# Kernel optimization log

Measured on AMD Instinct MI355X. Metric: run time of the kernel, lower is better.

## Reference

```python
import jax, jax.numpy as jnp
import numpy as np

N = 100000
HEADS = 4
NHID = 32


def _gat_conv(x, src, dst, W, a_src, a_dst, b):
    # x: [N, Fin]; src/dst: [E'] (self-loops already appended)
    h = (x @ W).reshape(N, HEADS, NHID)                      # [N, H, D]
    al_src = jnp.einsum('nhd,hd->nh', h, a_src)              # [N, H]
    al_dst = jnp.einsum('nhd,hd->nh', h, a_dst)
    e = jax.nn.leaky_relu(al_src[src] + al_dst[dst], 0.2)    # [E', H]
    # segment softmax over incoming edges of each destination node
    m = jax.ops.segment_max(e, dst, num_segments=N)          # [N, H]
    ex = jnp.exp(e - m[dst])
    s = jax.ops.segment_sum(ex, dst, num_segments=N)         # [N, H]
    alpha = ex / (s[dst] + 1e-16)                            # [E', H]
    msg = h[src] * alpha[:, :, None]                         # [E', H, D]
    out = jax.ops.segment_sum(msg, dst, num_segments=N)      # [N, H, D]
    return out.reshape(N, HEADS * NHID) + b


def setup_inputs() -> dict:
    key = jax.random.key(0)
    ks = jax.random.split(key, 16)
    E = 1600000
    NFEAT, NCLASS = 128, 10
    width = HEADS * NHID  # 128
    sc = 0.1
    inp = {
        'x': jax.random.normal(ks[0], (N, NFEAT), jnp.float32),
        'edge_index': jax.random.randint(ks[1], (2, E), 0, N, jnp.int64)
            if jax.config.jax_enable_x64 else jax.random.randint(ks[1], (2, E), 0, N, jnp.int32),
        'W0': jax.random.normal(ks[2], (NFEAT, width), jnp.float32) * sc,
        'a_src0': jax.random.normal(ks[3], (HEADS, NHID), jnp.float32) * sc,
        'a_dst0': jax.random.normal(ks[4], (HEADS, NHID), jnp.float32) * sc,
        'b0': jnp.zeros((width,), jnp.float32),
        'W1': jax.random.normal(ks[5], (width, width), jnp.float32) * sc,
        'a_src1': jax.random.normal(ks[6], (HEADS, NHID), jnp.float32) * sc,
        'a_dst1': jax.random.normal(ks[7], (HEADS, NHID), jnp.float32) * sc,
        'b1': jnp.zeros((width,), jnp.float32),
        'W2': jax.random.normal(ks[8], (width, width), jnp.float32) * sc,
        'a_src2': jax.random.normal(ks[9], (HEADS, NHID), jnp.float32) * sc,
        'a_dst2': jax.random.normal(ks[10], (HEADS, NHID), jnp.float32) * sc,
        'b2': jnp.zeros((width,), jnp.float32),
        'fc_W': jax.random.normal(ks[11], (width, NCLASS), jnp.float32) * sc,
        'fc_b': jnp.zeros((NCLASS,), jnp.float32),
    }
    return inp


def reference(x, edge_index, W0, a_src0, a_dst0, b0, W1, a_src1, a_dst1, b1,
              W2, a_src2, a_dst2, b2, fc_W, fc_b):
    # PyG GATConv default add_self_loops=True
    loops = jnp.arange(N, dtype=edge_index.dtype)
    src = jnp.concatenate([edge_index[0], loops])
    dst = jnp.concatenate([edge_index[1], loops])
    h = x
    for (W, a_s, a_d, b) in ((W0, a_src0, a_dst0, b0),
                             (W1, a_src1, a_dst1, b1),
                             (W2, a_src2, a_dst2, b2)):
        h = jax.nn.elu(_gat_conv(h, src, dst, W, a_s, a_d, b))
        # F.dropout(training=False) -> identity
    logits = h @ fc_W + fc_b
    return jax.nn.log_softmax(logits, axis=1)
```

## Files before the change

kernel.cpp:

```cpp
#include <hip/hip_runtime.h>
#include <math.h>

#define NN 100000
#define FEAT 128
#define NHEAD 4
#define BSH 9
#define BNODES 512
#define NBUCK 196
#define BCAP 16384
#define PA_EPT 16
#define GTILES 6250
#define GEMMB 512
#define HSTRIDE 136
#define SRCMASK 0x1FFFF

typedef unsigned int uint;
typedef unsigned short ushort;
typedef __attribute__((ext_vector_type(8))) short short8;
typedef __attribute__((ext_vector_type(4))) float fx4;

__device__ __forceinline__ float lrelu(float v) { return v > 0.f ? v : 0.2f * v; }

__device__ __forceinline__ ushort f2bf(float f) {
    uint u = __float_as_uint(f);
    return (ushort)((u + 0x7fffu + ((u >> 16) & 1u)) >> 16);
}
__device__ __forceinline__ float bf_lo(uint u) { return __uint_as_float(u << 16); }
__device__ __forceinline__ float bf_hi(uint u) { return __uint_as_float(u & 0xffff0000u); }

__device__ __forceinline__ short8 pack8f(const float* p) {
    float4 a = *(const float4*)p, b = *(const float4*)(p + 4);
    short8 v;
    v[0] = (short)f2bf(a.x); v[1] = (short)f2bf(a.y);
    v[2] = (short)f2bf(a.z); v[3] = (short)f2bf(a.w);
    v[4] = (short)f2bf(b.x); v[5] = (short)f2bf(b.y);
    v[6] = (short)f2bf(b.z); v[7] = (short)f2bf(b.w);
    return v;
}

template <bool FP32IN>
__device__ __forceinline__ void gemm_body(
    const void* __restrict__ in, const float* __restrict__ W,
    const float* __restrict__ a_src, const float* __restrict__ a_dst,
    ushort* __restrict__ hbf, float* __restrict__ al_s, float* __restrict__ al_d,
    int bid, int gridn)
{
    __shared__ __align__(16) ushort WA[FEAT * FEAT];
    __shared__ __align__(16) ushort HS[4][16 * HSTRIDE];
    const int t = threadIdx.x;
    for (int idx = t; idx < FEAT * FEAT; idx += 256) {
        int k = idx >> 7, m = idx & 127;
        int mt = m >> 4, kt = k >> 5, qq = (k >> 3) & 3, j = k & 7;
        int ln = qq * 16 + (m & 15);
        WA[((mt * 4 + kt) * 64 + ln) * 8 + j] = f2bf(W[idx]);
    }
    __syncthreads();

    const int wv = t >> 6, lane = t & 63;
    const int node_l = lane & 15, q = lane >> 4;

    short8 afr[8][4];
    #pragma unroll
    for (int mt = 0; mt < 8; ++mt)
        #pragma unroll
        for (int kt = 0; kt < 4; ++kt)
            afr[mt][kt] = *(const short8*)&WA[((mt * 4 + kt) * 64 + lane) * 8];

    const ushort* inbf = (const ushort*)in;
    const float*  inf  = (const float*)in;

    for (int tile = bid * 4 + wv; tile < GTILES; tile += gridn * 4) {
        const int n0 = tile * 16;
        short8 b0, b1, b2, b3;
        if (FP32IN) {
            const float* rf = inf + (size_t)(n0 + node_l) * FEAT + q * 8;
            b0 = pack8f(rf);
            b1 = pack8f(rf + 32);
            b2 = pack8f(rf + 64);
            b3 = pack8f(rf + 96);
        } else {
            const ushort* rowp = inbf + (size_t)(n0 + node_l) * FEAT + q * 8;
            b0 = *(const short8*)(rowp);
            b1 = *(const short8*)(rowp + 32);
            b2 = *(const short8*)(rowp + 64);
            b3 = *(const short8*)(rowp + 96);
        }
        fx4 zero = {0.f, 0.f, 0.f, 0.f};
        fx4 acc[8];
        #pragma unroll
        for (int mt = 0; mt < 8; ++mt) acc[mt] = zero;
        #pragma unroll
        for (int kt = 0; kt < 4; ++kt) {
            short8 b = (kt == 0) ? b0 : (kt == 1) ? b1 : (kt == 2) ? b2 : b3;
            #pragma unroll
            for (int mt = 0; mt < 8; ++mt)
                acc[mt] = __builtin_amdgcn_mfma_f32_16x16x32_bf16(afr[mt][kt], b, acc[mt], 0, 0, 0);
        }
        float ps[4] = {0.f, 0.f, 0.f, 0.f};
        float pd[4] = {0.f, 0.f, 0.f, 0.f};
        #pragma unroll
        for (int mt = 0; mt < 8; ++mt) {
            float4 as4 = *(const float4*)(a_src + mt * 16 + q * 4);
            float4 ad4 = *(const float4*)(a_dst + mt * 16 + q * 4);
            ps[mt >> 1] += acc[mt][0] * as4.x + acc[mt][1] * as4.y + acc[mt][2] * as4.z + acc[mt][3] * as4.w;
            pd[mt >> 1] += acc[mt][0] * ad4.x + acc[mt][1] * ad4.y + acc[mt][2] * ad4.z + acc[mt][3] * ad4.w;
            ushort4 hv;
            hv.x = f2bf(acc[mt][0]); hv.y = f2bf(acc[mt][1]);
            hv.z = f2bf(acc[mt][2]); hv.w = f2bf(acc[mt][3]);
            *(ushort4*)&HS[wv][node_l * HSTRIDE + mt * 16 + q * 4] = hv;
        }
        #pragma unroll
        for (int h = 0; h < 4; ++h) {
            ps[h] += __shfl_xor(ps[h], 16); ps[h] += __shfl_xor(ps[h], 32);
            pd[h] += __shfl_xor(pd[h], 16); pd[h] += __shfl_xor(pd[h], 32);
        }
        float vs = (q == 0) ? ps[0] : (q == 1) ? ps[1] : (q == 2) ? ps[2] : ps[3];
        float vd = (q == 0) ? pd[0] : (q == 1) ? pd[1] : (q == 2) ? pd[2] : pd[3];
        al_s[(n0 + node_l) * 4 + q] = vs;
        al_d[(n0 + node_l) * 4 + q] = vd;
        #pragma unroll
        for (int it = 0; it < 4; ++it) {
            int fi = it * 64 + lane;
            int row = fi >> 4, colc = fi & 15;
            short8 v = *(const short8*)&HS[wv][row * HSTRIDE + colc * 8];
            *(short8*)(hbf + (size_t)n0 * FEAT + (size_t)fi * 8) = v;
        }
    }
}

__device__ __forceinline__ void phaseA_body(
    const int* __restrict__ ei, int E, int* bcursor, uint* __restrict__ pairs, int bid)
{
    __shared__ int lh[NBUCK], lb[NBUCK];
    int t = threadIdx.x;
    if (t < NBUCK) lh[t] = 0;
    __syncthreads();
    int base = bid * (256 * PA_EPT) + t;
    int s[PA_EPT], d[PA_EPT];
    #pragma unroll
    for (int k = 0; k < PA_EPT; ++k) {
        int i = base + k * 256;
        if (i < E)            { s[k] = ei[i]; d[k] = ei[E + i]; }
        else if (i < E + NN)  { s[k] = i - E; d[k] = s[k]; }
        else                  { s[k] = 0; d[k] = -1; }
        if (d[k] >= 0) atomicAdd(&lh[d[k] >> BSH], 1);
    }
    __syncthreads();
    if (t < NBUCK) {
        int c = lh[t];
        lb[t] = c ? atomicAdd(&bcursor[t], c) : 0;
        lh[t] = 0;
    }
    __syncthreads();
    #pragma unroll
    for (int k = 0; k < PA_EPT; ++k) {
        if (d[k] >= 0) {
            int b = d[k] >> BSH;
            int off = atomicAdd(&lh[b], 1);
            pairs[lb[b] + off] = ((uint)(d[k] & (BNODES - 1)) << 17) | (uint)s[k];
        }
    }
}

__global__ __launch_bounds__(256, 2) void gemm_mfma_kernel(
    const void* __restrict__ in, const float* __restrict__ W,
    const float* __restrict__ a_src, const float* __restrict__ a_dst,
    ushort* __restrict__ hbf, float* __restrict__ al_s, float* __restrict__ al_d)
{
    gemm_body<false>(in, W, a_src, a_dst, hbf, al_s, al_d, blockIdx.x, GEMMB);
}

__global__ __launch_bounds__(256, 2) void gemm0_phaseA_kernel(
    const float* __restrict__ x, const float* __restrict__ W,
    const float* __restrict__ a_src, const float* __restrict__ a_dst,
    ushort* __restrict__ hbf, float* __restrict__ al_s, float* __restrict__ al_d,
    const int* __restrict__ ei, int E, int* bcursor, uint* __restrict__ pairs)
{
    if (blockIdx.x < GEMMB)
        gemm_body<true>(x, W, a_src, a_dst, hbf, al_s, al_d, blockIdx.x, GEMMB);
    else
        phaseA_body(ei, E, bcursor, pairs, blockIdx.x - GEMMB);
}


__global__ __launch_bounds__(256) void bucket_hist_kernel(
    const int* __restrict__ ei, int E, int* bsize)
{
    __shared__ int lh[NBUCK];
    int t = threadIdx.x;
    if (t < NBUCK) lh[t] = 0;
    __syncthreads();
    int stride = gridDim.x * 256;
    for (int i = blockIdx.x * 256 + t; i < E + NN; i += stride) {
        int d = (i < E) ? ei[E + i] : (i - E);
        atomicAdd(&lh[d >> BSH], 1);
    }
    __syncthreads();
    if (t < NBUCK && lh[t]) atomicAdd(&bsize[t], lh[t]);
}

__global__ __launch_bounds__(256) void bucket_scan_kernel(
    const int* __restrict__ bsize, int* bbase, int* bcursor)
{
    __shared__ int sm[256];
    int t = threadIdx.x;
    int v = (t < NBUCK) ? bsize[t] : 0;
    sm[t] = v;
    __syncthreads();
    #pragma unroll
    for (int off = 1; off < 256; off <<= 1) {
        int x = (t >= off) ? sm[t - off] : 0;
        __syncthreads();
        sm[t] += x;
        __syncthreads();
    }
    if (t < NBUCK) {
        int excl = sm[t] - v;
        bbase[t] = excl;
        bcursor[t] = excl;
    }
    if (t == 255) bbase[NBUCK] = sm[255];
}

__global__ __launch_bounds__(256) void phaseB_kernel(
    const uint* __restrict__ pairs, const int* __restrict__ bbase,
    int* __restrict__ row_ptr, int* __restrict__ colidx, int EP)
{
    __shared__ int nh[BNODES];
    __shared__ int ex[BNODES];
    __shared__ int ss[256];
    __shared__ int img[BCAP];
    int b = blockIdx.x, t = threadIdx.x;
    int node0 = b << BSH;
    int nend = min(NN - node0, BNODES);
    int pb = bbase[b], pe = bbase[b + 1];
    int span = pe - pb;
    for (int j = t; j < BNODES; j += 256) nh[j] = 0;
    __syncthreads();
    for (int i = t; i < span; i += 256)
        atomicAdd(&nh[pairs[pb + i] >> 17], 1);
    __syncthreads();
    int v0 = nh[2 * t], v1 = nh[2 * t + 1];
    int psc = v0 + v1;
    ss[t] = psc;
    __syncthreads();
    #pragma unroll
    for (int off = 1; off < 256; off <<= 1) {
        int x = (t >= off) ? ss[t - off] : 0;
        __syncthreads();
        ss[t] += x;
        __syncthreads();
    }
    int ep = ss[t] - psc;
    ex[2 * t] = ep;
    ex[2 * t + 1] = ep + v0;
    __syncthreads();
    for (int j = t; j < nend; j += 256) row_ptr[node0 + j] = pb + ex[j];
    if (b == NBUCK - 1 && t == 0) row_ptr[NN] = EP;
    for (int j = t; j < BNODES; j += 256) nh[j] = ex[j];
    __syncthreads();
    if (span <= BCAP) {
        for (int i = t; i < span; i += 256) {
            uint p = pairs[pb + i];
            int pos = atomicAdd(&nh[p >> 17], 1);
            img[pos] = (int)(p & SRCMASK);
        }
        __syncthreads();
        for (int i = t; i < span; i += 256) colidx[pb + i] = img[i];
    } else {
        for (int i = t; i < span; i += 256) {
            uint p = pairs[pb + i];
            int pos = atomicAdd(&nh[p >> 17], 1);
            colidx[pb + pos] = (int)(p & SRCMASK);
        }
    }
}

#define AGGR_STEP(hv, wgt)                                                    \
    a0 = fmaf(wgt, bf_lo(hv.x), a0); a1 = fmaf(wgt, bf_hi(hv.x), a1);        \
    a2 = fmaf(wgt, bf_lo(hv.y), a2); a3 = fmaf(wgt, bf_hi(hv.y), a3);        \
    a4 = fmaf(wgt, bf_lo(hv.z), a4); a5 = fmaf(wgt, bf_hi(hv.z), a5);        \
    a6 = fmaf(wgt, bf_lo(hv.w), a6); a7 = fmaf(wgt, bf_hi(hv.w), a7);

#define PROC4(cv)                                                             \
    {                                                                         \
        int s0 = cv.x, s1 = cv.y, s2 = cv.z, s3 = cv.w;                       \
        float w0 = __expf(lrelu(al_s[s0*4 + head] + ald_h));                  \
        float w1 = __expf(lrelu(al_s[s1*4 + head] + ald_h));                  \
        float w2 = __expf(lrelu(al_s[s2*4 + head] + ald_h));                  \
        float w3 = __expf(lrelu(al_s[s3*4 + head] + ald_h));                  \
        uint4 h0 = ((const uint4*)(hbf + (size_t)s0 * FEAT))[lane];           \
        uint4 h1 = ((const uint4*)(hbf + (size_t)s1 * FEAT))[lane];           \
        uint4 h2 = ((const uint4*)(hbf + (size_t)s2 * FEAT))[lane];           \
        uint4 h3 = ((const uint4*)(hbf + (size_t)s3 * FEAT))[lane];           \
        ssum += (w0 + w1) + (w2 + w3);                                        \
        AGGR_STEP(h0, w0) AGGR_STEP(h1, w1) AGGR_STEP(h2, w2) AGGR_STEP(h3, w3) \
    }

template <bool LAST>
__global__ __launch_bounds__(256) void aggr_csr_kernel(
    const int* __restrict__ row_ptr, const int* __restrict__ colidx,
    const ushort* __restrict__ hbf, const float* __restrict__ al_s,
    const float* __restrict__ al_d, const float* __restrict__ bias,
    ushort* __restrict__ outbf,
    const float* __restrict__ fcW, const float* __restrict__ fcb,
    float* __restrict__ logout)
{
    __shared__ float WT[10][FEAT];
    __shared__ float bl[10];
    int t = threadIdx.x;
    if (LAST) {
        for (int i = t; i < FEAT * 10; i += 256) {
            int k = i / 10, c = i % 10;
            WT[c][k] = fcW[i];
        }
        if (t < 10) bl[t] = fcb[t];
        __syncthreads();
    }
    int node = blockIdx.x * 16 + (t >> 4);
    int lane = t & 15;
    int head = lane >> 2;
    float ald_h = al_d[node * 4 + head];
    int beg = row_ptr[node], end = row_ptr[node + 1];

    float ssum = 0.f;
    float a0=0.f,a1=0.f,a2=0.f,a3=0.f,a4=0.f,a5=0.f,a6=0.f,a7=0.f;

    int p = beg;
    int4 ca;
    if (p + 4 <= end) ca = *(const int4*)&colidx[p];
    while (p + 8 <= end) {
        int4 na = *(const int4*)&colidx[p + 4];
        PROC4(ca)
        ca = na;
        p += 4;
    }
    if (p + 4 <= end) { PROC4(ca) p += 4; }
    for (; p < end; ++p) {
        int sn = colidx[p];
        float wq = __expf(lrelu(al_s[sn*4 + head] + ald_h));
        uint4 hv = ((const uint4*)(hbf + (size_t)sn * FEAT))[lane];
        ssum += wq;
        AGGR_STEP(hv, wq)
    }
    float inv = 1.f / (ssum + 1e-16f);
    const float* bp = bias + lane * 8;
    float o[8] = {a0,a1,a2,a3,a4,a5,a6,a7};
    #pragma unroll
    for (int k = 0; k < 8; ++k) {
        float v = o[k] * inv + bp[k];
        o[k] = v > 0.f ? v : __expf(v) - 1.f;
    }
    if (!LAST) {
        uint4 u;
        u.x = (uint)f2bf(o[0]) | ((uint)f2bf(o[1]) << 16);
        u.y = (uint)f2bf(o[2]) | ((uint)f2bf(o[3]) << 16);
        u.z = (uint)f2bf(o[4]) | ((uint)f2bf(o[5]) << 16);
        u.w = (uint)f2bf(o[6]) | ((uint)f2bf(o[7]) << 16);
        ((uint4*)(outbf + (size_t)node * FEAT))[lane] = u;
    } else {
        float lg[10];
        #pragma unroll
        for (int c = 0; c < 10; ++c) {
            const float* wr = &WT[c][lane * 8];
            float4 wa = *(const float4*)(wr);
            float4 wb = *(const float4*)(wr + 4);
            float acc = fmaf(o[0], wa.x, fmaf(o[1], wa.y, fmaf(o[2], wa.z, o[3] * wa.w)));
            acc = fmaf(o[4], wb.x, fmaf(o[5], wb.y, fmaf(o[6], wb.z, fmaf(o[7], wb.w, acc))));
            lg[c] = acc;
        }
        #pragma unroll
        for (int c = 0; c < 10; ++c) {
            lg[c] += __shfl_xor(lg[c], 1, 16);
            lg[c] += __shfl_xor(lg[c], 2, 16);
            lg[c] += __shfl_xor(lg[c], 4, 16);
            lg[c] += __shfl_xor(lg[c], 8, 16);
        }
        if (lane == 0) {
            float mx = -1e30f;
            #pragma unroll
            for (int c = 0; c < 10; ++c) { lg[c] += bl[c]; mx = fmaxf(mx, lg[c]); }
            float se = 0.f;
            #pragma unroll
            for (int c = 0; c < 10; ++c) se += __expf(lg[c] - mx);
            float lse = mx + __logf(se);
            float2* op = (float2*)(logout + (size_t)node * 10);
            #pragma unroll
            for (int c = 0; c < 5; ++c)
                op[c] = make_float2(lg[2*c] - lse, lg[2*c + 1] - lse);
        }
    }
}

extern "C" void kernel_launch(void* const* d_in, const int* in_sizes, int n_in,
                              void* d_out, int out_size, void* d_ws, size_t ws_size,
                              hipStream_t stream)
{
    const float* x   = (const float*)d_in[0];
    const int*   ei  = (const int*)d_in[1];
    const float* W[3]   = {(const float*)d_in[2], (const float*)d_in[6],  (const float*)d_in[10]};
    const float* asr[3] = {(const float*)d_in[3], (const float*)d_in[7],  (const float*)d_in[11]};
    const float* ads[3] = {(const float*)d_in[4], (const float*)d_in[8],  (const float*)d_in[12]};
    const float* bs[3]  = {(const float*)d_in[5], (const float*)d_in[9],  (const float*)d_in[13]};
    const float* fcW = (const float*)d_in[14];
    const float* fcb = (const float*)d_in[15];
    const int E  = in_sizes[1] / 2;
    const int EP = E + NN;

    ushort* hbf  = (ushort*)d_ws;
    ushort* ybf  = hbf + (size_t)NN * FEAT;
    float* als   = (float*)(ybf + (size_t)NN * FEAT);
    float* ald   = als + (size_t)NN * NHEAD;
    int* row_ptr = (int*)(ald + (size_t)NN * NHEAD);
    int* bsize   = row_ptr + NN + 1;
    int* bbase   = bsize + NBUCK;
    int* bcursor = bbase + NBUCK + 1;
    uint* pairs  = (uint*)(bcursor + NBUCK);
    int* colidx  = (int*)(pairs + (size_t)EP);

    const int pab = (EP + 256 * PA_EPT - 1) / (256 * PA_EPT);

    hipMemsetAsync(bsize, 0, NBUCK * sizeof(int), stream);
    bucket_hist_kernel<<<1024, 256, 0, stream>>>(ei, E, bsize);
    bucket_scan_kernel<<<1, 256, 0, stream>>>(bsize, bbase, bcursor);

    gemm0_phaseA_kernel<<<GEMMB + pab, 256, 0, stream>>>(
        x, W[0], asr[0], ads[0], hbf, als, ald, ei, E, bcursor, pairs);
    phaseB_kernel<<<NBUCK, 256, 0, stream>>>(pairs, bbase, row_ptr, colidx, EP);

    aggr_csr_kernel<false><<<(NN + 15) / 16, 256, 0, stream>>>(
        row_ptr, colidx, hbf, als, ald, bs[0], ybf, nullptr, nullptr, nullptr);

    gemm_mfma_kernel<<<GEMMB, 256, 0, stream>>>(ybf, W[1], asr[1], ads[1], hbf, als, ald);
    aggr_csr_kernel<false><<<(NN + 15) / 16, 256, 0, stream>>>(
        row_ptr, colidx, hbf, als, ald, bs[1], ybf, nullptr, nullptr, nullptr);

    gemm_mfma_kernel<<<GEMMB, 256, 0, stream>>>(ybf, W[2], asr[2], ads[2], hbf, als, ald);
    aggr_csr_kernel<true><<<(NN + 15) / 16, 256, 0, stream>>>(
        row_ptr, colidx, hbf, als, ald, bs[2], nullptr, fcW, fcb, (float*)d_out);
}
```

Before: 478.8 us.

## Double-buffer neighbor gathers and share edge weights via lane shuffles

```diff
diff --git a/kernel.cpp b/kernel.cpp
--- a/kernel.cpp
+++ b/kernel.cpp
@@ -282,19 +282,26 @@
     a4 = fmaf(wgt, bf_lo(hv.z), a4); a5 = fmaf(wgt, bf_hi(hv.z), a5);        \
     a6 = fmaf(wgt, bf_lo(hv.w), a6); a7 = fmaf(wgt, bf_hi(hv.w), a7);
 
-#define PROC4(cv)                                                             \
+#define GATHER4(c, hv, av)                                                    \
     {                                                                         \
-        int s0 = cv.x, s1 = cv.y, s2 = cv.z, s3 = cv.w;                       \
-        float w0 = __expf(lrelu(al_s[s0*4 + head] + ald_h));                  \
-        float w1 = __expf(lrelu(al_s[s1*4 + head] + ald_h));                  \
-        float w2 = __expf(lrelu(al_s[s2*4 + head] + ald_h));                  \
-        float w3 = __expf(lrelu(al_s[s3*4 + head] + ald_h));                  \
-        uint4 h0 = ((const uint4*)(hbf + (size_t)s0 * FEAT))[lane];           \
-        uint4 h1 = ((const uint4*)(hbf + (size_t)s1 * FEAT))[lane];           \
-        uint4 h2 = ((const uint4*)(hbf + (size_t)s2 * FEAT))[lane];           \
-        uint4 h3 = ((const uint4*)(hbf + (size_t)s3 * FEAT))[lane];           \
+        int sx = (sub == 0) ? c.x : (sub == 1) ? c.y : (sub == 2) ? c.z : c.w;\
+        av = al_s[sx * 4 + head];                                             \
+        hv[0] = ((const uint4*)(hbf + (size_t)c.x * FEAT))[lane];             \
+        hv[1] = ((const uint4*)(hbf + (size_t)c.y * FEAT))[lane];             \
+        hv[2] = ((const uint4*)(hbf + (size_t)c.z * FEAT))[lane];             \
+        hv[3] = ((const uint4*)(hbf + (size_t)c.w * FEAT))[lane];             \
+    }
+
+#define ACCUM4(hv, av)                                                        \
+    {                                                                         \
+        float ww = __expf(lrelu(av + ald_h));                                 \
+        float w0 = __shfl(ww, qbase | 0, 16);                                 \
+        float w1 = __shfl(ww, qbase | 1, 16);                                 \
+        float w2 = __shfl(ww, qbase | 2, 16);                                 \
+        float w3 = __shfl(ww, qbase | 3, 16);                                 \
         ssum += (w0 + w1) + (w2 + w3);                                        \
-        AGGR_STEP(h0, w0) AGGR_STEP(h1, w1) AGGR_STEP(h2, w2) AGGR_STEP(h3, w3) \
+        AGGR_STEP(hv[0], w0) AGGR_STEP(hv[1], w1)                             \
+        AGGR_STEP(hv[2], w2) AGGR_STEP(hv[3], w3)                             \
     }
 
 template <bool LAST>
@@ -320,29 +327,49 @@
     int node = blockIdx.x * 16 + (t >> 4);
     int lane = t & 15;
     int head = lane >> 2;
+    const int sub = lane & 3;
+    const int qbase = lane & 12;
     float ald_h = al_d[node * 4 + head];
     int beg = row_ptr[node], end = row_ptr[node + 1];
 
     float ssum = 0.f;
     float a0=0.f,a1=0.f,a2=0.f,a3=0.f,a4=0.f,a5=0.f,a6=0.f,a7=0.f;
 
-    int p = beg;
-    int4 ca;
-    if (p + 4 <= end) ca = *(const int4*)&colidx[p];
-    while (p + 8 <= end) {
-        int4 na = *(const int4*)&colidx[p + 4];
-        PROC4(ca)
-        ca = na;
-        p += 4;
-    }
-    if (p + 4 <= end) { PROC4(ca) p += 4; }
-    for (; p < end; ++p) {
+    const int nb = (end - beg) >> 2;
+    int4 c0, c1;
+    uint4 h0[4], h1[4];
+    float av0 = 0.f, av1 = 0.f;
+    if (nb >= 1) { c0 = *(const int4*)&colidx[beg];     GATHER4(c0, h0, av0) }
+    if (nb >= 2) { c1 = *(const int4*)&colidx[beg + 4]; GATHER4(c1, h1, av1) }
+    int i = 0;
+    for (; i + 3 < nb; i += 2) {
+        int4 cn0 = *(const int4*)&colidx[beg + (i + 2) * 4];
+        int4 cn1 = *(const int4*)&colidx[beg + (i + 3) * 4];
+        ACCUM4(h0, av0)
+        GATHER4(cn0, h0, av0)
+        ACCUM4(h1, av1)
+        GATHER4(cn1, h1, av1)
+    }
+    if (i + 2 < nb) {
+        int4 cn0 = *(const int4*)&colidx[beg + (i + 2) * 4];
+        ACCUM4(h0, av0)
+        GATHER4(cn0, h0, av0)
+        ACCUM4(h1, av1)
+        ACCUM4(h0, av0)
+    } else if (i + 1 < nb) {
+        ACCUM4(h0, av0)
+        ACCUM4(h1, av1)
+    } else if (i < nb) {
+        ACCUM4(h0, av0)
+    }
+    for (int p = beg + nb * 4; p < end; ++p) {
         int sn = colidx[p];
         float wq = __expf(lrelu(al_s[sn*4 + head] + ald_h));
         uint4 hv = ((const uint4*)(hbf + (size_t)sn * FEAT))[lane];
         ssum += wq;
         AGGR_STEP(hv, wq)
     }
+
     float inv = 1.f / (ssum + 1e-16f);
     const float* bp = bias + lane * 8;
     float o[8] = {a0,a1,a2,a3,a4,a5,a6,a7};
```

Result: slower. 490.4 us (+2.4%).

## Use one-tile-per-wave GEMM grid and unroll aggregation gather to 8 edges

Applied to the files above, without the earlier changes.

```diff
diff --git a/kernel.cpp b/kernel.cpp
--- a/kernel.cpp
+++ b/kernel.cpp
@@ -10,8 +10,7 @@
 #define BCAP 16384
 #define PA_EPT 16
 #define GTILES 6250
-#define GEMMB 512
-#define HSTRIDE 136
+#define GEMMB 1563
 #define SRCMASK 0x1FFFF
 
 typedef unsigned int uint;
@@ -43,35 +42,20 @@
     const void* __restrict__ in, const float* __restrict__ W,
     const float* __restrict__ a_src, const float* __restrict__ a_dst,
     ushort* __restrict__ hbf, float* __restrict__ al_s, float* __restrict__ al_d,
-    int bid, int gridn)
+    int bid)
 {
     __shared__ __align__(16) ushort WA[FEAT * FEAT];
-    __shared__ __align__(16) ushort HS[4][16 * HSTRIDE];
     const int t = threadIdx.x;
-    for (int idx = t; idx < FEAT * FEAT; idx += 256) {
-        int k = idx >> 7, m = idx & 127;
-        int mt = m >> 4, kt = k >> 5, qq = (k >> 3) & 3, j = k & 7;
-        int ln = qq * 16 + (m & 15);
-        WA[((mt * 4 + kt) * 64 + ln) * 8 + j] = f2bf(W[idx]);
-    }
-    __syncthreads();
-
-    const int wv = t >> 6, lane = t & 63;
+    const int lane = t & 63;
     const int node_l = lane & 15, q = lane >> 4;
-
-    short8 afr[8][4];
-    #pragma unroll
-    for (int mt = 0; mt < 8; ++mt)
-        #pragma unroll
-        for (int kt = 0; kt < 4; ++kt)
-            afr[mt][kt] = *(const short8*)&WA[((mt * 4 + kt) * 64 + lane) * 8];
-
+    const int tile = bid * 4 + (t >> 6);
+    const bool valid = tile < GTILES;
+    const int n0 = tile * 16;
+
+    short8 b0, b1, b2, b3;
     const ushort* inbf = (const ushort*)in;
     const float*  inf  = (const float*)in;
-
-    for (int tile = bid * 4 + wv; tile < GTILES; tile += gridn * 4) {
-        const int n0 = tile * 16;
-        short8 b0, b1, b2, b3;
+    if (valid) {
         if (FP32IN) {
             const float* rf = inf + (size_t)(n0 + node_l) * FEAT + q * 8;
             b0 = pack8f(rf);
@@ -85,47 +69,53 @@
             b2 = *(const short8*)(rowp + 64);
             b3 = *(const short8*)(rowp + 96);
         }
-        fx4 zero = {0.f, 0.f, 0.f, 0.f};
-        fx4 acc[8];
-        #pragma unroll
-        for (int mt = 0; mt < 8; ++mt) acc[mt] = zero;
-        #pragma unroll
-        for (int kt = 0; kt < 4; ++kt) {
-            short8 b = (kt == 0) ? b0 : (kt == 1) ? b1 : (kt == 2) ? b2 : b3;
-            #pragma unroll
-            for (int mt = 0; mt < 8; ++mt)
-                acc[mt] = __builtin_amdgcn_mfma_f32_16x16x32_bf16(afr[mt][kt], b, acc[mt], 0, 0, 0);
-        }
-        float ps[4] = {0.f, 0.f, 0.f, 0.f};
-        float pd[4] = {0.f, 0.f, 0.f, 0.f};
+    }
+
+    for (int idx = t; idx < FEAT * FEAT; idx += 256) {
+        int k = idx >> 7, m = idx & 127;
+        int mt = m >> 4, kt = k >> 5, qq = (k >> 3) & 3, j = k & 7;
+        int ln = qq * 16 + (m & 15);
+        WA[((mt * 4 + kt) * 64 + ln) * 8 + j] = f2bf(W[idx]);
+    }
+    __syncthreads();
+    if (!valid) return;
+
+    fx4 zero = {0.f, 0.f, 0.f, 0.f};
+    fx4 acc[8];
+    #pragma unroll
+    for (int mt = 0; mt < 8; ++mt) acc[mt] = zero;
+    #pragma unroll
+    for (int kt = 0; kt < 4; ++kt) {
+        short8 b = (kt == 0) ? b0 : (kt == 1) ? b1 : (kt == 2) ? b2 : b3;
         #pragma unroll
         for (int mt = 0; mt < 8; ++mt) {
-            float4 as4 = *(const float4*)(a_src + mt * 16 + q * 4);
-            float4 ad4 = *(const float4*)(a_dst + mt * 16 + q * 4);
-            ps[mt >> 1] += acc[mt][0] * as4.x + acc[mt][1] * as4.y + acc[mt][2] * as4.z + acc[mt][3] * as4.w;
-            pd[mt >> 1] += acc[mt][0] * ad4.x + acc[mt][1] * ad4.y + acc[mt][2] * ad4.z + acc[mt][3] * ad4.w;
-            ushort4 hv;
-            hv.x = f2bf(acc[mt][0]); hv.y = f2bf(acc[mt][1]);
-            hv.z = f2bf(acc[mt][2]); hv.w = f2bf(acc[mt][3]);
-            *(ushort4*)&HS[wv][node_l * HSTRIDE + mt * 16 + q * 4] = hv;
-        }
-        #pragma unroll
-        for (int h = 0; h < 4; ++h) {
-            ps[h] += __shfl_xor(ps[h], 16); ps[h] += __shfl_xor(ps[h], 32);
-            pd[h] += __shfl_xor(pd[h], 16); pd[h] += __shfl_xor(pd[h], 32);
-        }
-        float vs = (q == 0) ? ps[0] : (q == 1) ? ps[1] : (q == 2) ? ps[2] : ps[3];
-        float vd = (q == 0) ? pd[0] : (q == 1) ? pd[1] : (q == 2) ? pd[2] : pd[3];
-        al_s[(n0 + node_l) * 4 + q] = vs;
-        al_d[(n0 + node_l) * 4 + q] = vd;
-        #pragma unroll
-        for (int it = 0; it < 4; ++it) {
-            int fi = it * 64 + lane;
-            int row = fi >> 4, colc = fi & 15;
-            short8 v = *(const short8*)&HS[wv][row * HSTRIDE + colc * 8];
-            *(short8*)(hbf + (size_t)n0 * FEAT + (size_t)fi * 8) = v;
-        }
-    }
+            short8 a = *(const short8*)&WA[((mt * 4 + kt) * 64 + lane) * 8];
+            acc[mt] = __builtin_amdgcn_mfma_f32_16x16x32_bf16(a, b, acc[mt], 0, 0, 0);
+        }
+    }
+
+    float ps[4] = {0.f, 0.f, 0.f, 0.f};
+    float pd[4] = {0.f, 0.f, 0.f, 0.f};
+    #pragma unroll
+    for (int mt = 0; mt < 8; ++mt) {
+        float4 as4 = *(const float4*)(a_src + mt * 16 + q * 4);
+        float4 ad4 = *(const float4*)(a_dst + mt * 16 + q * 4);
+        ps[mt >> 1] += acc[mt][0] * as4.x + acc[mt][1] * as4.y + acc[mt][2] * as4.z + acc[mt][3] * as4.w;
+        pd[mt >> 1] += acc[mt][0] * ad4.x + acc[mt][1] * ad4.y + acc[mt][2] * ad4.z + acc[mt][3] * ad4.w;
+        ushort4 hv;
+        hv.x = f2bf(acc[mt][0]); hv.y = f2bf(acc[mt][1]);
+        hv.z = f2bf(acc[mt][2]); hv.w = f2bf(acc[mt][3]);
+        *(ushort4*)(hbf + (size_t)(n0 + node_l) * FEAT + mt * 16 + q * 4) = hv;
+    }
+    #pragma unroll
+    for (int h = 0; h < 4; ++h) {
+        ps[h] += __shfl_xor(ps[h], 16); ps[h] += __shfl_xor(ps[h], 32);
+        pd[h] += __shfl_xor(pd[h], 16); pd[h] += __shfl_xor(pd[h], 32);
+    }
+    float vs = (q == 0) ? ps[0] : (q == 1) ? ps[1] : (q == 2) ? ps[2] : ps[3];
+    float vd = (q == 0) ? pd[0] : (q == 1) ? pd[1] : (q == 2) ? pd[2] : pd[3];
+    al_s[(n0 + node_l) * 4 + q] = vs;
+    al_d[(n0 + node_l) * 4 + q] = vd;
 }
 
 __device__ __forceinline__ void phaseA_body(
@@ -167,7 +157,7 @@
     const float* __restrict__ a_src, const float* __restrict__ a_dst,
     ushort* __restrict__ hbf, float* __restrict__ al_s, float* __restrict__ al_d)
 {
-    gemm_body<false>(in, W, a_src, a_dst, hbf, al_s, al_d, blockIdx.x, GEMMB);
+    gemm_body<false>(in, W, a_src, a_dst, hbf, al_s, al_d, blockIdx.x);
 }
 
 __global__ __launch_bounds__(256, 2) void gemm0_phaseA_kernel(
@@ -177,7 +167,7 @@
     const int* __restrict__ ei, int E, int* bcursor, uint* __restrict__ pairs)
 {
     if (blockIdx.x < GEMMB)
-        gemm_body<true>(x, W, a_src, a_dst, hbf, al_s, al_d, blockIdx.x, GEMMB);
+        gemm_body<true>(x, W, a_src, a_dst, hbf, al_s, al_d, blockIdx.x);
     else
         phaseA_body(ei, E, bcursor, pairs, blockIdx.x - GEMMB);
 }
@@ -297,6 +287,31 @@
         AGGR_STEP(h0, w0) AGGR_STEP(h1, w1) AGGR_STEP(h2, w2) AGGR_STEP(h3, w3) \
     }
 
+#define PROC8(cva, cvb)                                                       \
+    {                                                                         \
+        int s0 = cva.x, s1 = cva.y, s2 = cva.z, s3 = cva.w;                   \
+        int s4 = cvb.x, s5 = cvb.y, s6 = cvb.z, s7 = cvb.w;                   \
+        uint4 h0 = ((const uint4*)(hbf + (size_t)s0 * FEAT))[lane];           \
+        uint4 h1 = ((const uint4*)(hbf + (size_t)s1 * FEAT))[lane];           \
+        uint4 h2 = ((const uint4*)(hbf + (size_t)s2 * FEAT))[lane];           \
+        uint4 h3 = ((const uint4*)(hbf + (size_t)s3 * FEAT))[lane];           \
+        uint4 h4 = ((const uint4*)(hbf + (size_t)s4 * FEAT))[lane];           \
+        uint4 h5 = ((const uint4*)(hbf + (size_t)s5 * FEAT))[lane];           \
+        uint4 h6 = ((const uint4*)(hbf + (size_t)s6 * FEAT))[lane];           \
+        uint4 h7 = ((const uint4*)(hbf + (size_t)s7 * FEAT))[lane];           \
+        float w0 = __expf(lrelu(al_s[s0*4 + head] + ald_h));                  \
+        float w1 = __expf(lrelu(al_s[s1*4 + head] + ald_h));                  \
+        float w2 = __expf(lrelu(al_s[s2*4 + head] + ald_h));                  \
+        float w3 = __expf(lrelu(al_s[s3*4 + head] + ald_h));                  \
+        float w4 = __expf(lrelu(al_s[s4*4 + head] + ald_h));                  \
+        float w5 = __expf(lrelu(al_s[s5*4 + head] + ald_h));                  \
+        float w6 = __expf(lrelu(al_s[s6*4 + head] + ald_h));                  \
+        float w7 = __expf(lrelu(al_s[s7*4 + head] + ald_h));                  \
+        ssum += ((w0 + w1) + (w2 + w3)) + ((w4 + w5) + (w6 + w7));            \
+        AGGR_STEP(h0, w0) AGGR_STEP(h1, w1) AGGR_STEP(h2, w2) AGGR_STEP(h3, w3) \
+        AGGR_STEP(h4, w4) AGGR_STEP(h5, w5) AGGR_STEP(h6, w6) AGGR_STEP(h7, w7) \
+    }
+
 template <bool LAST>
 __global__ __launch_bounds__(256) void aggr_csr_kernel(
     const int* __restrict__ row_ptr, const int* __restrict__ colidx,
@@ -327,15 +342,24 @@
     float a0=0.f,a1=0.f,a2=0.f,a3=0.f,a4=0.f,a5=0.f,a6=0.f,a7=0.f;
 
     int p = beg;
-    int4 ca;
-    if (p + 4 <= end) ca = *(const int4*)&colidx[p];
-    while (p + 8 <= end) {
-        int4 na = *(const int4*)&colidx[p + 4];
-        PROC4(ca)
-        ca = na;
+    int4 ca, cb;
+    if (p + 8 <= end) {
+        ca = *(const int4*)&colidx[p];
+        cb = *(const int4*)&colidx[p + 4];
+    }
+    while (p + 16 <= end) {
+        int4 na = *(const int4*)&colidx[p + 8];
+        int4 nb = *(const int4*)&colidx[p + 12];
+        PROC8(ca, cb)
+        ca = na; cb = nb;
+        p += 8;
+    }
+    if (p + 8 <= end) { PROC8(ca, cb) p += 8; }
+    if (p + 4 <= end) {
+        int4 c4 = *(const int4*)&colidx[p];
+        PROC4(c4)
         p += 4;
     }
-    if (p + 4 <= end) { PROC4(ca) p += 4; }
     for (; p < end; ++p) {
         int sn = colidx[p];
         float wq = __expf(lrelu(al_s[sn*4 + head] + ald_h));
@@ -343,6 +367,7 @@
         ssum += wq;
         AGGR_STEP(hv, wq)
     }
+
     float inv = 1.f / (ssum + 1e-16f);
     const float* bp = bias + lane * 8;
     float o[8] = {a0,a1,a2,a3,a4,a5,a6,a7};
```

Result: slower. 494.4 us (+3.2%).
